# Performance work log

Measured on AMD Instinct MI355X. Metric: run time of the kernel, lower is better.

The kernel has to match this reference:

```python
import jax, jax.numpy as jnp
import numpy as np

IN_SIZE = 1024
CLASSES = 7
N = 50000
LN_EPS = 1e-5


def _chain(x, w, b, g, beta):
    # Linear -> (Dropout=identity at eval) -> LayerNorm -> GELU(exact erf)
    h = x @ w.T + b
    mu = jnp.mean(h, axis=-1, keepdims=True)
    var = jnp.var(h, axis=-1, keepdims=True)
    h = (h - mu) / jnp.sqrt(var + LN_EPS) * g + beta
    return jax.nn.gelu(h, approximate=False)


def setup_inputs() -> dict:
    key = jax.random.key(0)
    ks = jax.random.split(key, 16)
    d = IN_SIZE
    std = 1.0 / np.sqrt(d)
    inp = {
        "features": jax.random.normal(ks[0], (N, d), jnp.float32),
        "c": jax.random.normal(ks[1], (N, CLASSES), jnp.float32),
        "key_w": jax.random.uniform(ks[2], (d, d), jnp.float32, -std, std),
        "key_b": jax.random.uniform(ks[3], (d,), jnp.float32, -std, std),
        "key_g": jnp.ones((d,), jnp.float32),
        "key_beta": jnp.zeros((d,), jnp.float32),
        "query_w": jax.random.uniform(ks[4], (d, d), jnp.float32, -std, std),
        "query_b": jax.random.uniform(ks[5], (d,), jnp.float32, -std, std),
        "query_g": jnp.ones((d,), jnp.float32),
        "query_beta": jnp.zeros((d,), jnp.float32),
        "value_w": jax.random.uniform(ks[6], (d, d), jnp.float32, -std, std),
        "value_b": jax.random.uniform(ks[7], (d,), jnp.float32, -std, std),
        "value_g": jnp.ones((d,), jnp.float32),
        "value_beta": jnp.zeros((d,), jnp.float32),
        "head_w": jax.random.uniform(ks[8], (CLASSES, CLASSES, d), jnp.float32, -1.0 / np.sqrt(CLASSES * d), 1.0 / np.sqrt(CLASSES * d)),
        "head_b": jax.random.uniform(ks[9], (CLASSES,), jnp.float32, -1.0 / np.sqrt(CLASSES * d), 1.0 / np.sqrt(CLASSES * d)),
    }
    return inp


def reference(features, c, key_w, key_b, key_g, key_beta,
              query_w, query_b, query_g, query_beta,
              value_w, value_b, value_g, value_beta,
              head_w, head_b):
    K = _chain(features, key_w, key_b, key_g, key_beta)          # [N, d]
    V = _chain(K, value_w, value_b, value_g, value_beta)         # [N, d]
    Q = _chain(K, query_w, query_b, query_g, query_beta)         # [N, d]
    # critical (top-scoring) instance per class
    top_idx = jnp.argmax(c, axis=0)                              # [classes]
    m_feats = K[top_idx]                                         # [classes, d]
    q_max = _chain(m_feats, query_w, query_b, query_g, query_beta)  # [classes, d]
    A = Q @ q_max.T                                              # [N, classes]
    A = jax.nn.softmax(A / jnp.sqrt(jnp.float32(Q.shape[1])), axis=0)
    B = A.T @ V                                                  # [classes, d]
    # Conv1d(classes, classes, kernel_size=d) on [1, classes, d] -> full contraction
    C = jnp.einsum('ik,oik->o', B, head_w) + head_b              # [classes]
    C = C.reshape(1, -1)
    return (C, A, B.reshape(1, CLASSES, -1))
```

## Files before the change

### kernel.cpp

```cpp
#include <hip/hip_runtime.h>


typedef unsigned short u16;
typedef __attribute__((ext_vector_type(8))) short          bf16x8;
typedef __attribute__((ext_vector_type(8))) unsigned short u16x8;
typedef __attribute__((ext_vector_type(4))) unsigned short u16x4;
typedef __attribute__((ext_vector_type(4))) float          f32x4;

#define DDIM  1024
#define NROWS 50000
#define MP    50048
#define NCLS  7
#define MPD4  12512

__device__ __forceinline__ u16 f2bf(float f) {
  unsigned u = __float_as_uint(f);
  u = (u + 0x7FFFu + ((u >> 16) & 1u)) >> 16;
  return (u16)u;
}
__device__ __forceinline__ float bf2f(u16 h) {
  return __uint_as_float(((unsigned)h) << 16);
}
__device__ __forceinline__ float gelu(float x) {
  return 0.5f * x * (1.0f + erff(x * 0.70710678118654752f));
}

__device__ __forceinline__ void load16_lds(const u16* g, u16* l) {
  __builtin_amdgcn_global_load_lds(
      (const __attribute__((address_space(1))) unsigned int*)(const void*)g,
      (__attribute__((address_space(3))) unsigned int*)(void*)l, 16, 0, 0);
}

__global__ __launch_bounds__(256) void k_convert(const float* __restrict__ src,
                                                 u16* __restrict__ dst,
                                                 int rows_total, int rows_valid) {
  const size_t total = (size_t)rows_total * DDIM / 8;
  const size_t stride = (size_t)gridDim.x * blockDim.x;
  for (size_t i = (size_t)blockIdx.x * blockDim.x + threadIdx.x; i < total; i += stride) {
    const size_t e = i * 8;
    const int row = (int)(e >> 10);
    u16x8 o = {0, 0, 0, 0, 0, 0, 0, 0};
    if (row < rows_valid) {
      const float4* p = (const float4*)(src + e);
      float4 f0 = p[0], f1 = p[1];
      o[0] = f2bf(f0.x); o[1] = f2bf(f0.y); o[2] = f2bf(f0.z); o[3] = f2bf(f0.w);
      o[4] = f2bf(f1.x); o[5] = f2bf(f1.y); o[6] = f2bf(f1.z); o[7] = f2bf(f1.w);
    }
    *(u16x8*)(dst + e) = o;
  }
}

__global__ __launch_bounds__(256) void k_convw(const float* __restrict__ kw,
                                               const float* __restrict__ vw,
                                               const float* __restrict__ qw,
                                               u16* __restrict__ Wk,
                                               u16* __restrict__ Wvq) {
  const int w = blockIdx.x >> 7;
  const int b = blockIdx.x & 127;
  const float* src = (w == 0) ? kw : (w == 1) ? vw : qw;
  u16* dst = (w == 0) ? Wk : (Wvq + (size_t)(w - 1) * DDIM * DDIM);
  for (int i = b * 256 + threadIdx.x; i < DDIM * DDIM / 8; i += 128 * 256) {
    const float4* p = (const float4*)(src + (size_t)i * 8);
    float4 f0 = p[0], f1 = p[1];
    u16x8 o;
    o[0] = f2bf(f0.x); o[1] = f2bf(f0.y); o[2] = f2bf(f0.z); o[3] = f2bf(f0.w);
    o[4] = f2bf(f1.x); o[5] = f2bf(f1.y); o[6] = f2bf(f1.z); o[7] = f2bf(f1.w);
    *(u16x8*)(dst + (size_t)i * 8) = o;
  }
}

__global__ __launch_bounds__(256) void k_gemm_bt(const u16* __restrict__ A,
                                                 const u16* __restrict__ B,
                                                 u16* __restrict__ C,
                                                 int lnn, int ldc) {
  __shared__ __align__(16) u16 As[128 * 32];
  __shared__ __align__(16) u16 Bs[128 * 32];
  const int tid  = threadIdx.x;
  const int lane = tid & 63;
  const int cpx = gridDim.x >> 3;
  const int v   = (blockIdx.x & 7) * cpx + (blockIdx.x >> 3);
  const int m0 = (v >> lnn) * 128;
  const int n0 = (v & ((1 << lnn) - 1)) * 128;
  const int wid = tid >> 6;
  const int wr = (wid >> 1) * 64;
  const int wc = (wid & 1) * 64;

  const int rA = tid >> 2;
  const int cA = (tid & 3) * 8;
  const u16* Ap0 = A + (size_t)(m0 + rA) * DDIM + cA;
  const u16* Ap1 = Ap0 + (size_t)64 * DDIM;
  const u16* Bp0 = B + (size_t)(n0 + rA) * DDIM + cA;
  const u16* Bp1 = Bp0 + (size_t)64 * DDIM;
  const int wbase = wid * 64;
  u16* AsD0 = &As[(wbase)       * 8];
  u16* AsD1 = &As[(wbase + 256) * 8];
  u16* BsD0 = &Bs[(wbase)       * 8];
  u16* BsD1 = &Bs[(wbase + 256) * 8];

  f32x4 acc[4][4] = {};
  const int fr = lane & 15;
  const int kh = (lane >> 4) * 8;

  for (int k0 = 0; k0 < DDIM; k0 += 32) {
    __syncthreads();
    load16_lds(Ap0 + k0, AsD0);
    load16_lds(Ap1 + k0, AsD1);
    load16_lds(Bp0 + k0, BsD0);
    load16_lds(Bp1 + k0, BsD1);
    __syncthreads();
    bf16x8 a[4], b[4];
#pragma unroll
    for (int i = 0; i < 4; ++i) a[i] = *(const bf16x8*)&As[(wr + i * 16 + fr) * 32 + kh];
#pragma unroll
    for (int j = 0; j < 4; ++j) b[j] = *(const bf16x8*)&Bs[(wc + j * 16 + fr) * 32 + kh];
#pragma unroll
    for (int i = 0; i < 4; ++i)
#pragma unroll
      for (int j = 0; j < 4; ++j)
        acc[i][j] = __builtin_amdgcn_mfma_f32_16x16x32_bf16(a[i], b[j], acc[i][j], 0, 0, 0);
  }

  const int orow = (lane >> 4) * 4;
  const int ocol = lane & 15;
#pragma unroll
  for (int i = 0; i < 4; ++i)
#pragma unroll
    for (int j = 0; j < 4; ++j) {
      const size_t base = (size_t)(m0 + wr + i * 16 + orow) * ldc + (n0 + wc + j * 16 + ocol);
#pragma unroll
      for (int r = 0; r < 4; ++r)
        C[base + (size_t)r * ldc] = f2bf(acc[i][j][r]);
    }
}

__global__ __launch_bounds__(256) void k_ln_k(const u16* __restrict__ h,
                                              const float* __restrict__ bias,
                                              const float* __restrict__ g,
                                              const float* __restrict__ beta,
                                              u16* __restrict__ out) {
  const int lane = threadIdx.x & 63;
  const int row = blockIdx.x * 4 + (threadIdx.x >> 6);
  const int c0 = lane * 8;
  u16x8* op0 = (u16x8*)(out + (size_t)row * DDIM + c0);
  u16x8* op1 = (u16x8*)(out + (size_t)row * DDIM + 512 + c0);
  if (row >= NROWS) {
    u16x8 z = {0, 0, 0, 0, 0, 0, 0, 0};
    *op0 = z; *op1 = z;
    return;
  }
  u16x8 h0 = *(const u16x8*)(h + (size_t)row * DDIM + c0);
  u16x8 h1 = *(const u16x8*)(h + (size_t)row * DDIM + 512 + c0);
  float4 a0 = *(const float4*)(bias + c0), a1 = *(const float4*)(bias + c0 + 4);
  float4 a2 = *(const float4*)(bias + 512 + c0), a3 = *(const float4*)(bias + 512 + c0 + 4);
  const float ba[8] = {a0.x, a0.y, a0.z, a0.w, a1.x, a1.y, a1.z, a1.w};
  const float bb[8] = {a2.x, a2.y, a2.z, a2.w, a3.x, a3.y, a3.z, a3.w};
  float v0[8], v1[8];
  float s1 = 0.f, s2 = 0.f;
#pragma unroll
  for (int e = 0; e < 8; ++e) {
    v0[e] = bf2f(h0[e]) + ba[e];
    v1[e] = bf2f(h1[e]) + bb[e];
    s1 += v0[e] + v1[e];
    s2 += v0[e] * v0[e] + v1[e] * v1[e];
  }
#pragma unroll
  for (int m = 1; m < 64; m <<= 1) {
    s1 += __shfl_xor(s1, m, 64);
    s2 += __shfl_xor(s2, m, 64);
  }
  const float mu = s1 * (1.0f / 1024.0f);
  const float var = s2 * (1.0f / 1024.0f) - mu * mu;
  const float rs = rsqrtf(var + 1e-5f);
  float4 g0 = *(const float4*)(g + c0), g1 = *(const float4*)(g + c0 + 4);
  float4 g2 = *(const float4*)(g + 512 + c0), g3 = *(const float4*)(g + 512 + c0 + 4);
  float4 t0 = *(const float4*)(beta + c0), t1 = *(const float4*)(beta + c0 + 4);
  float4 t2 = *(const float4*)(beta + 512 + c0), t3 = *(const float4*)(beta + 512 + c0 + 4);
  const float ga[8] = {g0.x, g0.y, g0.z, g0.w, g1.x, g1.y, g1.z, g1.w};
  const float gb[8] = {g2.x, g2.y, g2.z, g2.w, g3.x, g3.y, g3.z, g3.w};
  const float ta[8] = {t0.x, t0.y, t0.z, t0.w, t1.x, t1.y, t1.z, t1.w};
  const float tb[8] = {t2.x, t2.y, t2.z, t2.w, t3.x, t3.y, t3.z, t3.w};
  u16x8 o0, o1;
#pragma unroll
  for (int e = 0; e < 8; ++e) {
    o0[e] = f2bf(gelu((v0[e] - mu) * rs * ga[e] + ta[e]));
    o1[e] = f2bf(gelu((v1[e] - mu) * rs * gb[e] + tb[e]));
  }
  *op0 = o0; *op1 = o1;
}

__global__ __launch_bounds__(256) void k_qmax(const u16* __restrict__ K,
                                              const int* __restrict__ top,
                                              const u16* __restrict__ Wq,
                                              const float* __restrict__ qb,
                                              const float* __restrict__ qg,
                                              const float* __restrict__ qbeta,
                                              u16* __restrict__ qm) {
  __shared__ __align__(16) u16 krow[DDIM];
  __shared__ float w1[4], w2[4];
  const int t = threadIdx.x;
  const int j = blockIdx.x;
  const u16* src = K + (size_t)top[j] * DDIM;
  if (t < 128) *(u16x8*)&krow[t * 8] = *(const u16x8*)&src[t * 8];
  __syncthreads();
  float acc[4];
#pragma unroll
  for (int c = 0; c < 4; ++c) {
    const int col = t * 4 + c;
    const u16x8* wp = (const u16x8*)(Wq + (size_t)col * DDIM);
    float s = 0.f;
    for (int kc = 0; kc < 128; ++kc) {
      u16x8 wv = wp[kc];
      u16x8 kv = *(const u16x8*)&krow[kc * 8];
#pragma unroll
      for (int e = 0; e < 8; ++e) s += bf2f(kv[e]) * bf2f(wv[e]);
    }
    acc[c] = s + qb[col];
  }
  float s1 = acc[0] + acc[1] + acc[2] + acc[3];
  float s2 = acc[0] * acc[0] + acc[1] * acc[1] + acc[2] * acc[2] + acc[3] * acc[3];
#pragma unroll
  for (int m = 1; m < 64; m <<= 1) {
    s1 += __shfl_xor(s1, m, 64);
    s2 += __shfl_xor(s2, m, 64);
  }
  if ((t & 63) == 0) { w1[t >> 6] = s1; w2[t >> 6] = s2; }
  __syncthreads();
  s1 = w1[0] + w1[1] + w1[2] + w1[3];
  s2 = w2[0] + w2[1] + w2[2] + w2[3];
  const float mu = s1 * (1.0f / 1024.0f);
  const float var = s2 * (1.0f / 1024.0f) - mu * mu;
  const float rs = rsqrtf(var + 1e-5f);
#pragma unroll
  for (int c = 0; c < 4; ++c) {
    const int col = t * 4 + c;
    qm[(size_t)j * DDIM + col] = f2bf(gelu((acc[c] - mu) * rs * qg[col] + qbeta[col]));
  }
}

__global__ __launch_bounds__(256) void k_ln_vq(const u16* __restrict__ h,
                                               const float* __restrict__ v_b,
                                               const float* __restrict__ v_g,
                                               const float* __restrict__ v_beta,
                                               const float* __restrict__ q_b,
                                               const float* __restrict__ q_g,
                                               const float* __restrict__ q_beta,
                                               const u16* __restrict__ qm,
                                               u16* __restrict__ V,
                                               float* __restrict__ logits) {
  __shared__ __align__(16) u16 sqm[NCLS * DDIM];
  const int tid = threadIdx.x;
  const int lane = tid & 63;
  const int half = (blockIdx.x >= MPD4) ? 1 : 0;
  const int rb = half ? (blockIdx.x - MPD4) : blockIdx.x;
  const int row = rb * 4 + (tid >> 6);
  if (half) {
    for (int i = tid; i < NCLS * DDIM / 8; i += 256)
      *(u16x8*)&sqm[i * 8] = *(const u16x8*)&qm[i * 8];
    __syncthreads();
  }
  if (row >= NROWS) return;
  const float* bias = half ? q_b : v_b;
  const float* gain = half ? q_g : v_g;
  const float* bet  = half ? q_beta : v_beta;
  const int c0 = lane * 8;
  const u16* hp = h + (size_t)row * 2048 + (size_t)half * DDIM;
  u16x8 h0 = *(const u16x8*)(hp + c0);
  u16x8 h1 = *(const u16x8*)(hp + 512 + c0);
  float4 a0 = *(const float4*)(bias + c0), a1 = *(const float4*)(bias + c0 + 4);
  float4 a2 = *(const float4*)(bias + 512 + c0), a3 = *(const float4*)(bias + 512 + c0 + 4);
  const float ba[8] = {a0.x, a0.y, a0.z, a0.w, a1.x, a1.y, a1.z, a1.w};
  const float bb[8] = {a2.x, a2.y, a2.z, a2.w, a3.x, a3.y, a3.z, a3.w};
  float v0[8], v1[8];
  float s1 = 0.f, s2 = 0.f;
#pragma unroll
  for (int e = 0; e < 8; ++e) {
    v0[e] = bf2f(h0[e]) + ba[e];
    v1[e] = bf2f(h1[e]) + bb[e];
    s1 += v0[e] + v1[e];
    s2 += v0[e] * v0[e] + v1[e] * v1[e];
  }
#pragma unroll
  for (int m = 1; m < 64; m <<= 1) {
    s1 += __shfl_xor(s1, m, 64);
    s2 += __shfl_xor(s2, m, 64);
  }
  const float mu = s1 * (1.0f / 1024.0f);
  const float var = s2 * (1.0f / 1024.0f) - mu * mu;
  const float rs = rsqrtf(var + 1e-5f);
  float4 g0 = *(const float4*)(gain + c0), g1 = *(const float4*)(gain + c0 + 4);
  float4 g2 = *(const float4*)(gain + 512 + c0), g3 = *(const float4*)(gain + 512 + c0 + 4);
  float4 t0 = *(const float4*)(bet + c0), t1 = *(const float4*)(bet + c0 + 4);
  float4 t2 = *(const float4*)(bet + 512 + c0), t3 = *(const float4*)(bet + 512 + c0 + 4);
  const float ga[8] = {g0.x, g0.y, g0.z, g0.w, g1.x, g1.y, g1.z, g1.w};
  const float gb[8] = {g2.x, g2.y, g2.z, g2.w, g3.x, g3.y, g3.z, g3.w};
  const float ta[8] = {t0.x, t0.y, t0.z, t0.w, t1.x, t1.y, t1.z, t1.w};
  const float tb[8] = {t2.x, t2.y, t2.z, t2.w, t3.x, t3.y, t3.z, t3.w};
  float y0[8], y1[8];
#pragma unroll
  for (int e = 0; e < 8; ++e) {
    y0[e] = gelu((v0[e] - mu) * rs * ga[e] + ta[e]);
    y1[e] = gelu((v1[e] - mu) * rs * gb[e] + tb[e]);
  }
  if (half == 0) {
    u16x8 o0, o1;
#pragma unroll
    for (int e = 0; e < 8; ++e) { o0[e] = f2bf(y0[e]); o1[e] = f2bf(y1[e]); }
    *(u16x8*)(V + (size_t)row * DDIM + c0) = o0;
    *(u16x8*)(V + (size_t)row * DDIM + 512 + c0) = o1;
  } else {
#pragma unroll
    for (int j = 0; j < NCLS; ++j) {
      u16x8 m0 = *(const u16x8*)&sqm[j * DDIM + c0];
      u16x8 m1 = *(const u16x8*)&sqm[j * DDIM + 512 + c0];
      float p = 0.f;
#pragma unroll
      for (int e = 0; e < 8; ++e) p += y0[e] * bf2f(m0[e]) + y1[e] * bf2f(m1[e]);
#pragma unroll
      for (int m = 1; m < 64; m <<= 1) p += __shfl_xor(p, m, 64);
      if (lane == 0) logits[(size_t)row * NCLS + j] = p * 0.03125f;
    }
  }
}

__global__ __launch_bounds__(256) void k_arg1(const float* __restrict__ c,
                                              float* __restrict__ pv,
                                              int* __restrict__ pi) {
  __shared__ float sv[256 * NCLS];
  __shared__ int   si[256 * NCLS];
  const int t = threadIdx.x;
  float bv[NCLS]; int bi[NCLS];
#pragma unroll
  for (int j = 0; j < NCLS; ++j) { bv[j] = -3.4e38f; bi[j] = 0x7fffffff; }
  for (int n = blockIdx.x * 256 + t; n < NROWS; n += 128 * 256) {
#pragma unroll
    for (int j = 0; j < NCLS; ++j) {
      const float v = c[(size_t)n * NCLS + j];
      if (v > bv[j]) { bv[j] = v; bi[j] = n; }
    }
  }
#pragma unroll
  for (int j = 0; j < NCLS; ++j) { sv[t * NCLS + j] = bv[j]; si[t * NCLS + j] = bi[j]; }
  __syncthreads();
  for (int s = 128; s > 0; s >>= 1) {
    if (t < s) {
#pragma unroll
      for (int j = 0; j < NCLS; ++j) {
        const float v2 = sv[(t + s) * NCLS + j]; const int i2 = si[(t + s) * NCLS + j];
        const float v1 = sv[t * NCLS + j];       const int i1 = si[t * NCLS + j];
        if (v2 > v1 || (v2 == v1 && i2 < i1)) { sv[t * NCLS + j] = v2; si[t * NCLS + j] = i2; }
      }
    }
    __syncthreads();
  }
  if (t < NCLS) { pv[blockIdx.x * NCLS + t] = sv[t]; pi[blockIdx.x * NCLS + t] = si[t]; }
}

__global__ void k_arg2(const float* __restrict__ pv, const int* __restrict__ pi,
                       int* __restrict__ top) {
  __shared__ float sv[128 * NCLS];
  __shared__ int   si[128 * NCLS];
  const int t = threadIdx.x;
#pragma unroll
  for (int j = 0; j < NCLS; ++j) { sv[t * NCLS + j] = pv[t * NCLS + j]; si[t * NCLS + j] = pi[t * NCLS + j]; }
  __syncthreads();
  for (int s = 64; s > 0; s >>= 1) {
    if (t < s) {
#pragma unroll
      for (int j = 0; j < NCLS; ++j) {
        const float v2 = sv[(t + s) * NCLS + j]; const int i2 = si[(t + s) * NCLS + j];
        const float v1 = sv[t * NCLS + j];       const int i1 = si[t * NCLS + j];
        if (v2 > v1 || (v2 == v1 && i2 < i1)) { sv[t * NCLS + j] = v2; si[t * NCLS + j] = i2; }
      }
    }
    __syncthreads();
  }
  if (t < NCLS) top[t] = si[t];
}

__global__ __launch_bounds__(256) void k_cmax_part(const float* __restrict__ logits,
                                                   float* __restrict__ pout) {
  __shared__ float sm[256 * NCLS];
  const int tid = threadIdx.x;
  float m[NCLS];
#pragma unroll
  for (int j = 0; j < NCLS; ++j) m[j] = -3.4e38f;
  const size_t stride = (size_t)gridDim.x * 256;
  for (size_t n = (size_t)blockIdx.x * 256 + tid; n < NROWS; n += stride)
#pragma unroll
    for (int j = 0; j < NCLS; ++j) m[j] = fmaxf(m[j], logits[n * NCLS + j]);
#pragma unroll
  for (int j = 0; j < NCLS; ++j) sm[tid * NCLS + j] = m[j];
  __syncthreads();
  for (int s = 128; s > 0; s >>= 1) {
    if (tid < s)
#pragma unroll
      for (int j = 0; j < NCLS; ++j)
        sm[tid * NCLS + j] = fmaxf(sm[tid * NCLS + j], sm[(tid + s) * NCLS + j]);
    __syncthreads();
  }
  if (tid < NCLS) pout[blockIdx.x * NCLS + tid] = sm[tid];
}

__global__ void k_cmax_fin(const float* __restrict__ pin, float* __restrict__ M, int nparts) {
  const int tid = threadIdx.x;
  if (tid < NCLS) {
    float m = -3.4e38f;
    for (int b = 0; b < nparts; ++b) m = fmaxf(m, pin[b * NCLS + tid]);
    M[tid] = m;
  }
}

__global__ __launch_bounds__(256) void k_csum_part(const float* __restrict__ logits,
                                                   const float* __restrict__ M,
                                                   float* __restrict__ pout) {
  __shared__ float sm[256 * NCLS];
  __shared__ float sM[NCLS];
  const int tid = threadIdx.x;
  if (tid < NCLS) sM[tid] = M[tid];
  __syncthreads();
  float s[NCLS];
#pragma unroll
  for (int j = 0; j < NCLS; ++j) s[j] = 0.f;
  const size_t stride = (size_t)gridDim.x * 256;
  for (size_t n = (size_t)blockIdx.x * 256 + tid; n < NROWS; n += stride)
#pragma unroll
    for (int j = 0; j < NCLS; ++j) s[j] += expf(logits[n * NCLS + j] - sM[j]);
#pragma unroll
  for (int j = 0; j < NCLS; ++j) sm[tid * NCLS + j] = s[j];
  __syncthreads();
  for (int st = 128; st > 0; st >>= 1) {
    if (tid < st)
#pragma unroll
      for (int j = 0; j < NCLS; ++j) sm[tid * NCLS + j] += sm[(tid + st) * NCLS + j];
    __syncthreads();
  }
  if (tid < NCLS) pout[blockIdx.x * NCLS + tid] = sm[tid];
}

__global__ void k_csum_fin(const float* __restrict__ pin, float* __restrict__ S, int nparts) {
  const int tid = threadIdx.x;
  if (tid < NCLS) {
    float s = 0.f;
    for (int b = 0; b < nparts; ++b) s += pin[b * NCLS + tid];
    S[tid] = s;
  }
}

__global__ __launch_bounds__(256) void k_bpart(const float* __restrict__ logits,
                                               const float* __restrict__ M,
                                               const float* __restrict__ S,
                                               const u16* __restrict__ V,
                                               float* __restrict__ Aout,
                                               float* __restrict__ Pb) {
  __shared__ float sA[98 * NCLS];
  __shared__ float sM[NCLS], sR[NCLS];
  const int t = threadIdx.x;
  if (t < NCLS) { sM[t] = M[t]; sR[t] = 1.0f / S[t]; }
  __syncthreads();
  const int n0 = blockIdx.x * 98;
  int cnt = NROWS - n0;
  cnt = cnt < 0 ? 0 : (cnt > 98 ? 98 : cnt);
  for (int idx = t; idx < cnt * NCLS; idx += 256) {
    const int j = idx % NCLS;
    const float a = expf(logits[(size_t)n0 * NCLS + idx] - sM[j]) * sR[j];
    sA[idx] = a;
    Aout[(size_t)n0 * NCLS + idx] = a;
  }
  __syncthreads();
  float acc[NCLS][4] = {};
  for (int r = 0; r < cnt; ++r) {
    u16x4 vv = *(const u16x4*)&V[(size_t)(n0 + r) * DDIM + t * 4];
    const float f0 = bf2f(vv[0]), f1 = bf2f(vv[1]), f2 = bf2f(vv[2]), f3 = bf2f(vv[3]);
#pragma unroll
    for (int j = 0; j < NCLS; ++j) {
      const float a = sA[r * NCLS + j];
      acc[j][0] += a * f0; acc[j][1] += a * f1; acc[j][2] += a * f2; acc[j][3] += a * f3;
    }
  }
#pragma unroll
  for (int j = 0; j < NCLS; ++j) {
    f32x4 o = {acc[j][0], acc[j][1], acc[j][2], acc[j][3]};
    *(f32x4*)&Pb[((size_t)blockIdx.x * NCLS + j) * DDIM + t * 4] = o;
  }
}

__global__ void k_bred(const float* __restrict__ Pb, float* __restrict__ Bout) {
  const int idx = blockIdx.x * 256 + threadIdx.x;
  if (idx >= NCLS * DDIM) return;
  float s = 0.f;
  for (int p = 0; p < 512; ++p) s += Pb[(size_t)p * NCLS * DDIM + idx];
  Bout[idx] = s;
}

__global__ __launch_bounds__(256) void k_head(const float* __restrict__ Bmat,
                                              const float* __restrict__ hw,
                                              const float* __restrict__ hb,
                                              float* __restrict__ Cout) {
  const int o = blockIdx.x, t = threadIdx.x;
  float p = 0.f;
  for (int idx = t; idx < NCLS * DDIM; idx += 256)
    p += Bmat[idx] * hw[(size_t)o * NCLS * DDIM + idx];
#pragma unroll
  for (int m = 1; m < 64; m <<= 1) p += __shfl_xor(p, m, 64);
  __shared__ float w[4];
  if ((t & 63) == 0) w[t >> 6] = p;
  __syncthreads();
  if (t == 0) Cout[o] = w[0] + w[1] + w[2] + w[3] + hb[o];
}

extern "C" void kernel_launch(void* const* d_in, const int* in_sizes, int n_in,
                              void* d_out, int out_size, void* d_ws, size_t ws_size,
                              hipStream_t stream) {
  const float* features   = (const float*)d_in[0];
  const float* c_in       = (const float*)d_in[1];
  const float* key_w      = (const float*)d_in[2];
  const float* key_b      = (const float*)d_in[3];
  const float* key_g      = (const float*)d_in[4];
  const float* key_beta   = (const float*)d_in[5];
  const float* query_w    = (const float*)d_in[6];
  const float* query_b    = (const float*)d_in[7];
  const float* query_g    = (const float*)d_in[8];
  const float* query_beta = (const float*)d_in[9];
  const float* value_w    = (const float*)d_in[10];
  const float* value_b    = (const float*)d_in[11];
  const float* value_g    = (const float*)d_in[12];
  const float* value_beta = (const float*)d_in[13];
  const float* head_w     = (const float*)d_in[14];
  const float* head_b     = (const float*)d_in[15];

  char* ws = (char*)d_ws;
  const size_t SZB = (size_t)MP * DDIM * 2;
  u16* Xb   = (u16*)ws;
  u16* HbVQ = Xb;
  u16* HbK  = (u16*)(ws + SZB);
  u16* Kb   = (u16*)(ws + 2 * SZB);
  u16* Vb   = Kb;
  size_t off = 3 * SZB;
  u16* Wk  = (u16*)(ws + off); off += (size_t)DDIM * DDIM * 2;
  u16* Wvq = (u16*)(ws + off); off += (size_t)2 * DDIM * DDIM * 2;
  float* logits = (float*)(ws + off); off += ((size_t)NROWS * NCLS * 4 + 255) & ~(size_t)255;
  float* Pb  = (float*)(ws + off); off += (size_t)512 * NCLS * DDIM * 4;
  u16* qm    = (u16*)(ws + off); off += ((size_t)NCLS * DDIM * 2 + 255) & ~(size_t)255;
  float* Pmax = (float*)(ws + off); off += ((size_t)128 * NCLS * 4 + 255) & ~(size_t)255;
  float* Psum = (float*)(ws + off); off += ((size_t)128 * NCLS * 4 + 255) & ~(size_t)255;
  float* argv = (float*)(ws + off); off += ((size_t)128 * NCLS * 4 + 255) & ~(size_t)255;
  int*   argi = (int*)  (ws + off); off += ((size_t)128 * NCLS * 4 + 255) & ~(size_t)255;
  float* Mmax = (float*)(ws + off); off += 256;
  float* Ssum = (float*)(ws + off); off += 256;
  int*   top  = (int*)  (ws + off); off += 256;

  float* Cout = (float*)d_out;
  float* Aout = Cout + NCLS;
  float* Bout = Aout + (size_t)NROWS * NCLS;

  k_arg1<<<128, 256, 0, stream>>>(c_in, argv, argi);
  k_arg2<<<1, 128, 0, stream>>>(argv, argi, top);
  k_convert<<<2048, 256, 0, stream>>>(features, Xb, MP, NROWS);
  k_convw<<<384, 256, 0, stream>>>(key_w, value_w, query_w, Wk, Wvq);

  k_gemm_bt<<<3128, 256, 0, stream>>>(Xb, Wk, HbK, 3, 1024);
  k_ln_k<<<MPD4, 256, 0, stream>>>(HbK, key_b, key_g, key_beta, Kb);

  k_qmax<<<NCLS, 256, 0, stream>>>(Kb, top, Wvq + (size_t)DDIM * DDIM,
                                   query_b, query_g, query_beta, qm);

  k_gemm_bt<<<6256, 256, 0, stream>>>(Kb, Wvq, HbVQ, 4, 2048);
  k_ln_vq<<<2 * MPD4, 256, 0, stream>>>(HbVQ, value_b, value_g, value_beta,
                                        query_b, query_g, query_beta, qm, Vb, logits);

  k_cmax_part<<<128, 256, 0, stream>>>(logits, Pmax);
  k_cmax_fin<<<1, 32, 0, stream>>>(Pmax, Mmax, 128);
  k_csum_part<<<128, 256, 0, stream>>>(logits, Mmax, Psum);
  k_csum_fin<<<1, 32, 0, stream>>>(Psum, Ssum, 128);

  k_bpart<<<512, 256, 0, stream>>>(logits, Mmax, Ssum, Vb, Aout, Pb);
  k_bred<<<28, 256, 0, stream>>>(Pb, Bout);
  k_head<<<NCLS, 256, 0, stream>>>(Bout, head_w, head_b, Cout);
}
```

Before: 829.5 us.

## Multi-buffer GEMM LDS pipeline, derive q_max from Q GEMM rows, fold reduction kernels

The GEMM main loop now uses a 4-deep ring of LDS buffers, prefetching three k-tiles ahead and waiting with explicit vmcnt counts and a single barrier per step. The goal is to overlap global-to-LDS loads with MFMA work, at the cost of four times the LDS per block, which may lower occupancy. The q_max chain no longer runs its own matrix-vector product. It reads the already computed Q pre-activation rows at the argmax indices, with the argmax finalisation folded into that kernel. The max and sum finalisation kernels are merged into their consumers, which cuts several tiny launches.

```diff
diff --git a/kernel.cpp b/kernel.cpp
--- a/kernel.cpp
+++ b/kernel.cpp
@@ -73,8 +73,8 @@
                                                  const u16* __restrict__ B,
                                                  u16* __restrict__ C,
                                                  int lnn, int ldc) {
-  __shared__ __align__(16) u16 As[128 * 32];
-  __shared__ __align__(16) u16 Bs[128 * 32];
+  __shared__ __align__(16) u16 As[4][4096];
+  __shared__ __align__(16) u16 Bs[4][4096];
   const int tid  = threadIdx.x;
   const int lane = tid & 63;
   const int cpx = gridDim.x >> 3;
@@ -91,34 +91,49 @@
   const u16* Ap1 = Ap0 + (size_t)64 * DDIM;
   const u16* Bp0 = B + (size_t)(n0 + rA) * DDIM + cA;
   const u16* Bp1 = Bp0 + (size_t)64 * DDIM;
-  const int wbase = wid * 64;
-  u16* AsD0 = &As[(wbase)       * 8];
-  u16* AsD1 = &As[(wbase + 256) * 8];
-  u16* BsD0 = &Bs[(wbase)       * 8];
-  u16* BsD1 = &Bs[(wbase + 256) * 8];
+  const int wb8 = wid * 512;
 
   f32x4 acc[4][4] = {};
   const int fr = lane & 15;
   const int kh = (lane >> 4) * 8;
 
-  for (int k0 = 0; k0 < DDIM; k0 += 32) {
-    __syncthreads();
-    load16_lds(Ap0 + k0, AsD0);
-    load16_lds(Ap1 + k0, AsD1);
-    load16_lds(Bp0 + k0, BsD0);
-    load16_lds(Bp1 + k0, BsD1);
-    __syncthreads();
-    bf16x8 a[4], b[4];
-#pragma unroll
-    for (int i = 0; i < 4; ++i) a[i] = *(const bf16x8*)&As[(wr + i * 16 + fr) * 32 + kh];
-#pragma unroll
-    for (int j = 0; j < 4; ++j) b[j] = *(const bf16x8*)&Bs[(wc + j * 16 + fr) * 32 + kh];
-#pragma unroll
-    for (int i = 0; i < 4; ++i)
-#pragma unroll
-      for (int j = 0; j < 4; ++j)
-        acc[i][j] = __builtin_amdgcn_mfma_f32_16x16x32_bf16(a[i], b[j], acc[i][j], 0, 0, 0);
-  }
+#define STAGE_KT(KT) do { const int _b = (KT) & 3; const int _ko = (KT) * 32;  \
+    load16_lds(Ap0 + _ko, &As[_b][wb8]);                                       \
+    load16_lds(Ap1 + _ko, &As[_b][wb8 + 2048]);                                \
+    load16_lds(Bp0 + _ko, &Bs[_b][wb8]);                                       \
+    load16_lds(Bp1 + _ko, &Bs[_b][wb8 + 2048]); } while (0)
+
+#define COMPUTE_KT(KT) do { const int _b = (KT) & 3;                           \
+    const u16* _Ab = &As[_b][0]; const u16* _Bb = &Bs[_b][0];                  \
+    bf16x8 a[4], b[4];                                                         \
+    _Pragma("unroll") for (int i = 0; i < 4; ++i)                              \
+      a[i] = *(const bf16x8*)&_Ab[(wr + i * 16 + fr) * 32 + kh];               \
+    _Pragma("unroll") for (int j = 0; j < 4; ++j)                              \
+      b[j] = *(const bf16x8*)&_Bb[(wc + j * 16 + fr) * 32 + kh];               \
+    _Pragma("unroll") for (int i = 0; i < 4; ++i)                              \
+      _Pragma("unroll") for (int j = 0; j < 4; ++j)                            \
+        acc[i][j] = __builtin_amdgcn_mfma_f32_16x16x32_bf16(a[i], b[j],        \
+                                                            acc[i][j], 0, 0, 0); } while (0)
+
+  STAGE_KT(0); STAGE_KT(1); STAGE_KT(2);
+  asm volatile("s_waitcnt vmcnt(8)\n\ts_barrier" ::: "memory");
+
+#pragma unroll 4
+  for (int kt = 0; kt < 28; ++kt) {
+    STAGE_KT(kt + 3);
+    COMPUTE_KT(kt);
+    asm volatile("s_waitcnt vmcnt(8)\n\ts_barrier" ::: "memory");
+  }
+  STAGE_KT(31);
+  COMPUTE_KT(28);
+  asm volatile("s_waitcnt vmcnt(8)\n\ts_barrier" ::: "memory");
+  COMPUTE_KT(29);
+  asm volatile("s_waitcnt vmcnt(4)\n\ts_barrier" ::: "memory");
+  COMPUTE_KT(30);
+  asm volatile("s_waitcnt vmcnt(0)\n\ts_barrier" ::: "memory");
+  COMPUTE_KT(31);
+#undef STAGE_KT
+#undef COMPUTE_KT
 
   const int orow = (lane >> 4) * 4;
   const int ocol = lane & 15;
@@ -188,53 +203,57 @@
   *op0 = o0; *op1 = o1;
 }
 
-__global__ __launch_bounds__(256) void k_qmax(const u16* __restrict__ K,
-                                              const int* __restrict__ top,
-                                              const u16* __restrict__ Wq,
+__global__ __launch_bounds__(64) void k_qmax2(const float* __restrict__ argv,
+                                              const int* __restrict__ argi,
+                                              const u16* __restrict__ hvq,
                                               const float* __restrict__ qb,
                                               const float* __restrict__ qg,
                                               const float* __restrict__ qbeta,
                                               u16* __restrict__ qm) {
-  __shared__ __align__(16) u16 krow[DDIM];
-  __shared__ float w1[4], w2[4];
-  const int t = threadIdx.x;
   const int j = blockIdx.x;
-  const u16* src = K + (size_t)top[j] * DDIM;
-  if (t < 128) *(u16x8*)&krow[t * 8] = *(const u16x8*)&src[t * 8];
-  __syncthreads();
-  float acc[4];
-#pragma unroll
-  for (int c = 0; c < 4; ++c) {
-    const int col = t * 4 + c;
-    const u16x8* wp = (const u16x8*)(Wq + (size_t)col * DDIM);
-    float s = 0.f;
-    for (int kc = 0; kc < 128; ++kc) {
-      u16x8 wv = wp[kc];
-      u16x8 kv = *(const u16x8*)&krow[kc * 8];
-#pragma unroll
-      for (int e = 0; e < 8; ++e) s += bf2f(kv[e]) * bf2f(wv[e]);
-    }
-    acc[c] = s + qb[col];
-  }
-  float s1 = acc[0] + acc[1] + acc[2] + acc[3];
-  float s2 = acc[0] * acc[0] + acc[1] * acc[1] + acc[2] * acc[2] + acc[3] * acc[3];
+  const int lane = threadIdx.x;
+  float bv = -3.4e38f; int bi = 0x7fffffff;
+  for (int p = lane; p < 128; p += 64) {
+    const float v = argv[p * NCLS + j];
+    const int   i = argi[p * NCLS + j];
+    if (v > bv || (v == bv && i < bi)) { bv = v; bi = i; }
+  }
+#pragma unroll
+  for (int m = 1; m < 64; m <<= 1) {
+    const float ov = __shfl_xor(bv, m, 64);
+    const int   oi = __shfl_xor(bi, m, 64);
+    if (ov > bv || (ov == bv && oi < bi)) { bv = ov; bi = oi; }
+  }
+  const int row = bi;
+  const int c0 = lane * 8;
+  const u16* hp = hvq + (size_t)row * 2048 + DDIM;
+  u16x8 h0 = *(const u16x8*)(hp + c0);
+  u16x8 h1 = *(const u16x8*)(hp + 512 + c0);
+  float v0[8], v1[8];
+  float s1 = 0.f, s2 = 0.f;
+#pragma unroll
+  for (int e = 0; e < 8; ++e) {
+    v0[e] = bf2f(h0[e]) + qb[c0 + e];
+    v1[e] = bf2f(h1[e]) + qb[512 + c0 + e];
+    s1 += v0[e] + v1[e];
+    s2 += v0[e] * v0[e] + v1[e] * v1[e];
+  }
 #pragma unroll
   for (int m = 1; m < 64; m <<= 1) {
     s1 += __shfl_xor(s1, m, 64);
     s2 += __shfl_xor(s2, m, 64);
   }
-  if ((t & 63) == 0) { w1[t >> 6] = s1; w2[t >> 6] = s2; }
-  __syncthreads();
-  s1 = w1[0] + w1[1] + w1[2] + w1[3];
-  s2 = w2[0] + w2[1] + w2[2] + w2[3];
   const float mu = s1 * (1.0f / 1024.0f);
   const float var = s2 * (1.0f / 1024.0f) - mu * mu;
   const float rs = rsqrtf(var + 1e-5f);
-#pragma unroll
-  for (int c = 0; c < 4; ++c) {
-    const int col = t * 4 + c;
-    qm[(size_t)j * DDIM + col] = f2bf(gelu((acc[c] - mu) * rs * qg[col] + qbeta[col]));
-  }
+  u16x8 o0, o1;
+#pragma unroll
+  for (int e = 0; e < 8; ++e) {
+    o0[e] = f2bf(gelu((v0[e] - mu) * rs * qg[c0 + e] + qbeta[c0 + e]));
+    o1[e] = f2bf(gelu((v1[e] - mu) * rs * qg[512 + c0 + e] + qbeta[512 + c0 + e]));
+  }
+  *(u16x8*)(qm + (size_t)j * DDIM + c0) = o0;
+  *(u16x8*)(qm + (size_t)j * DDIM + 512 + c0) = o1;
 }
 
 __global__ __launch_bounds__(256) void k_ln_vq(const u16* __restrict__ h,
@@ -355,28 +374,6 @@
   if (t < NCLS) { pv[blockIdx.x * NCLS + t] = sv[t]; pi[blockIdx.x * NCLS + t] = si[t]; }
 }
 
-__global__ void k_arg2(const float* __restrict__ pv, const int* __restrict__ pi,
-                       int* __restrict__ top) {
-  __shared__ float sv[128 * NCLS];
-  __shared__ int   si[128 * NCLS];
-  const int t = threadIdx.x;
-#pragma unroll
-  for (int j = 0; j < NCLS; ++j) { sv[t * NCLS + j] = pv[t * NCLS + j]; si[t * NCLS + j] = pi[t * NCLS + j]; }
-  __syncthreads();
-  for (int s = 64; s > 0; s >>= 1) {
-    if (t < s) {
-#pragma unroll
-      for (int j = 0; j < NCLS; ++j) {
-        const float v2 = sv[(t + s) * NCLS + j]; const int i2 = si[(t + s) * NCLS + j];
-        const float v1 = sv[t * NCLS + j];       const int i1 = si[t * NCLS + j];
-        if (v2 > v1 || (v2 == v1 && i2 < i1)) { sv[t * NCLS + j] = v2; si[t * NCLS + j] = i2; }
-      }
-    }
-    __syncthreads();
-  }
-  if (t < NCLS) top[t] = si[t];
-}
-
 __global__ __launch_bounds__(256) void k_cmax_part(const float* __restrict__ logits,
                                                    float* __restrict__ pout) {
   __shared__ float sm[256 * NCLS];
@@ -401,22 +398,17 @@
   if (tid < NCLS) pout[blockIdx.x * NCLS + tid] = sm[tid];
 }
 
-__global__ void k_cmax_fin(const float* __restrict__ pin, float* __restrict__ M, int nparts) {
-  const int tid = threadIdx.x;
-  if (tid < NCLS) {
-    float m = -3.4e38f;
-    for (int b = 0; b < nparts; ++b) m = fmaxf(m, pin[b * NCLS + tid]);
-    M[tid] = m;
-  }
-}
-
 __global__ __launch_bounds__(256) void k_csum_part(const float* __restrict__ logits,
-                                                   const float* __restrict__ M,
+                                                   const float* __restrict__ Pmax,
                                                    float* __restrict__ pout) {
   __shared__ float sm[256 * NCLS];
   __shared__ float sM[NCLS];
   const int tid = threadIdx.x;
-  if (tid < NCLS) sM[tid] = M[tid];
+  if (tid < NCLS) {
+    float m = -3.4e38f;
+    for (int b = 0; b < 128; ++b) m = fmaxf(m, Pmax[b * NCLS + tid]);
+    sM[tid] = m;
+  }
   __syncthreads();
   float s[NCLS];
 #pragma unroll
@@ -437,25 +429,22 @@
   if (tid < NCLS) pout[blockIdx.x * NCLS + tid] = sm[tid];
 }
 
-__global__ void k_csum_fin(const float* __restrict__ pin, float* __restrict__ S, int nparts) {
-  const int tid = threadIdx.x;
-  if (tid < NCLS) {
-    float s = 0.f;
-    for (int b = 0; b < nparts; ++b) s += pin[b * NCLS + tid];
-    S[tid] = s;
-  }
-}
-
 __global__ __launch_bounds__(256) void k_bpart(const float* __restrict__ logits,
-                                               const float* __restrict__ M,
-                                               const float* __restrict__ S,
+                                               const float* __restrict__ Pmax,
+                                               const float* __restrict__ Psum,
                                                const u16* __restrict__ V,
                                                float* __restrict__ Aout,
                                                float* __restrict__ Pb) {
   __shared__ float sA[98 * NCLS];
   __shared__ float sM[NCLS], sR[NCLS];
   const int t = threadIdx.x;
-  if (t < NCLS) { sM[t] = M[t]; sR[t] = 1.0f / S[t]; }
+  if (t < NCLS) {
+    float m = -3.4e38f;
+    for (int b = 0; b < 128; ++b) m = fmaxf(m, Pmax[b * NCLS + t]);
+    float s = 0.f;
+    for (int b = 0; b < 128; ++b) s += Psum[b * NCLS + t];
+    sM[t] = m; sR[t] = 1.0f / s;
+  }
   __syncthreads();
   const int n0 = blockIdx.x * 98;
   int cnt = NROWS - n0;
@@ -545,35 +534,27 @@
   float* Psum = (float*)(ws + off); off += ((size_t)128 * NCLS * 4 + 255) & ~(size_t)255;
   float* argv = (float*)(ws + off); off += ((size_t)128 * NCLS * 4 + 255) & ~(size_t)255;
   int*   argi = (int*)  (ws + off); off += ((size_t)128 * NCLS * 4 + 255) & ~(size_t)255;
-  float* Mmax = (float*)(ws + off); off += 256;
-  float* Ssum = (float*)(ws + off); off += 256;
-  int*   top  = (int*)  (ws + off); off += 256;
 
   float* Cout = (float*)d_out;
   float* Aout = Cout + NCLS;
   float* Bout = Aout + (size_t)NROWS * NCLS;
 
   k_arg1<<<128, 256, 0, stream>>>(c_in, argv, argi);
-  k_arg2<<<1, 128, 0, stream>>>(argv, argi, top);
   k_convert<<<2048, 256, 0, stream>>>(features, Xb, MP, NROWS);
   k_convw<<<384, 256, 0, stream>>>(key_w, value_w, query_w, Wk, Wvq);
 
   k_gemm_bt<<<3128, 256, 0, stream>>>(Xb, Wk, HbK, 3, 1024);
   k_ln_k<<<MPD4, 256, 0, stream>>>(HbK, key_b, key_g, key_beta, Kb);
 
-  k_qmax<<<NCLS, 256, 0, stream>>>(Kb, top, Wvq + (size_t)DDIM * DDIM,
-                                   query_b, query_g, query_beta, qm);
-
   k_gemm_bt<<<6256, 256, 0, stream>>>(Kb, Wvq, HbVQ, 4, 2048);
+  k_qmax2<<<NCLS, 64, 0, stream>>>(argv, argi, HbVQ, query_b, query_g, query_beta, qm);
   k_ln_vq<<<2 * MPD4, 256, 0, stream>>>(HbVQ, value_b, value_g, value_beta,
                                         query_b, query_g, query_beta, qm, Vb, logits);
 
   k_cmax_part<<<128, 256, 0, stream>>>(logits, Pmax);
-  k_cmax_fin<<<1, 32, 0, stream>>>(Pmax, Mmax, 128);
-  k_csum_part<<<128, 256, 0, stream>>>(logits, Mmax, Psum);
-  k_csum_fin<<<1, 32, 0, stream>>>(Psum, Ssum, 128);
-
-  k_bpart<<<512, 256, 0, stream>>>(logits, Mmax, Ssum, Vb, Aout, Pb);
+  k_csum_part<<<128, 256, 0, stream>>>(logits, Pmax, Psum);
+
+  k_bpart<<<512, 256, 0, stream>>>(logits, Pmax, Psum, Vb, Aout, Pb);
   k_bred<<<28, 256, 0, stream>>>(Pb, Bout);
   k_head<<<NCLS, 256, 0, stream>>>(Bout, head_w, head_b, Cout);
 }
```

Measured after the change: 823.7 us. Within noise of the previous version (-0.7%).
